# Kernel optimization log

Hardware: AMD Instinct MI355X
Metric: run time of the kernel (lower is better)

The kernel has to match this reference:

```python
import jax, jax.numpy as jnp
import numpy as np

N, E = 50000, 800000
IN_C, HID, OUT_C = 128, 128, 64
EPS = 1e-5


def layer_norm(x, gamma, beta):
    mu = jnp.mean(x, axis=-1, keepdims=True)
    var = jnp.mean(jnp.square(x - mu), axis=-1, keepdims=True)
    return (x - mu) * jax.lax.rsqrt(var + EPS) * gamma + beta


def sage_conv(h, src, dst, W_l, b_l, W_r):
    # PyG SAGEConv (aggr='mean'): out = lin_l(mean_{j in N(i)} h_j) + lin_r(h_i)
    msg = h[src]                                                   # [E, HID] gather
    s = jax.ops.segment_sum(msg, dst, num_segments=N)              # [N, HID]
    cnt = jax.ops.segment_sum(jnp.ones((src.shape[0], 1), h.dtype), dst, num_segments=N)
    mean = s / jnp.maximum(cnt, 1.0)
    return mean @ W_l + b_l + h @ W_r


def setup_inputs() -> dict:
    key = jax.random.key(0)
    ks = jax.random.split(key, 12)
    sd_in = 1.0 / np.sqrt(IN_C)
    sd_h = 1.0 / np.sqrt(HID)
    return {
        "x": jax.random.normal(ks[0], (N, IN_C), jnp.float32),
        "edge_index": jax.random.randint(ks[1], (2, E), 0, N, jnp.int32),
        "edge_attr": jax.random.normal(ks[2], (E, IN_C), jnp.float32),
        "W_ne": jax.random.uniform(ks[3], (IN_C, HID), jnp.float32, -sd_in, sd_in),
        "b_ne": jax.random.uniform(ks[4], (HID,), jnp.float32, -sd_in, sd_in),
        "W_l": jax.random.uniform(ks[5], (HID, HID), jnp.float32, -sd_h, sd_h),
        "b_l": jax.random.uniform(ks[6], (HID,), jnp.float32, -sd_h, sd_h),
        "W_r": jax.random.uniform(ks[7], (HID, HID), jnp.float32, -sd_h, sd_h),
        "gamma": jnp.ones((HID,), jnp.float32),
        "beta": jnp.zeros((HID,), jnp.float32),
        "W_lin": jax.random.uniform(ks[8], (HID, OUT_C), jnp.float32, -sd_h, sd_h),
        "b_lin": jax.random.uniform(ks[9], (OUT_C,), jnp.float32, -sd_h, sd_h),
    }


def reference(x, edge_index, edge_attr, W_ne, b_ne, W_l, b_l, W_r, gamma, beta, W_lin, b_lin):
    src, dst = edge_index[0], edge_index[1]
    # node encoder
    h = x @ W_ne + b_ne
    # pre-conv with layers[0].conv
    h = sage_conv(h, src, dst, W_l, b_l, W_r)
    # layers[0] is unfixed: LN -> ReLU -> dropout(eval=id) -> conv -> residual
    r = layer_norm(h, gamma, beta)
    r = jax.nn.relu(r)
    h = sage_conv(r, src, dst, W_l, b_l, W_r) + h
    # layers[1:] are fixed -> identity
    # final norm/act/dropout(eval=id)/lin (reuses layers[0].norm/act)
    o = jax.nn.relu(layer_norm(h, gamma, beta))
    return o @ W_lin + b_lin
```

## Files before the change

### kernel.cpp

```cpp
#include <hip/hip_runtime.h>

typedef __attribute__((ext_vector_type(8))) short bf16x8;
typedef __attribute__((ext_vector_type(4))) float f32x4;

constexpr float LN_EPS = 1e-5f;

__device__ inline ushort f2bf(float f) {
  uint u = __float_as_uint(f);
  u += 0x7FFF + ((u >> 16) & 1);
  return (ushort)(u >> 16);
}
__device__ inline float bflo(uint u) { return __uint_as_float(u << 16); }
__device__ inline float bfhi(uint u) { return __uint_as_float(u & 0xFFFF0000u); }
__device__ inline uint pk2(float lo, float hi) { return (uint)f2bf(lo) | ((uint)f2bf(hi) << 16); }

struct Params {
  const float* x; const int* ei;
  const float *W_ne, *b_ne, *W_l, *b_l, *W_r, *gamma, *beta, *W_lin, *b_lin;
  float* out;
  ushort *Qbf, *H1, *Dbf, *xbf, *WAt, *WBt, *Wlt, *Wrt, *Wlint;
  signed char* Aq;
  float* Ascale;
  float *bA, *bB;
  int *cnt, *incl, *rowptr, *cursor, *bsums, *srclist;
  int N, E, nbS, nbT, nbE;
};


__global__ __launch_bounds__(256) void k_m1(Params p) {
  __shared__ float srow[128];
  const int tid = threadIdx.x, bid = blockIdx.x;
  if (bid < p.nbE) {
    int e = bid * 256 + tid;
    if (e < p.E) atomicAdd(&p.cnt[p.ei[p.E + e]], 1);
  } else if (bid < p.nbE + 129) {
    int blk = bid - p.nbE;
    const float* src = (blk < 128) ? (p.W_ne + blk * 128) : p.b_ne;
    if (tid < 128) srow[tid] = src[tid];
    __syncthreads();
    int col = tid & 127;
    const float* Wx = (tid < 128) ? p.W_l : p.W_r;
    float acc = 0.f;
#pragma unroll 8
    for (int k = 0; k < 128; ++k) acc = fmaf(srow[k], Wx[k * 128 + col], acc);
    if (blk < 128) {
      ushort* dst = (tid < 128) ? p.WAt : p.WBt;
      dst[col * 128 + blk] = f2bf(acc);
    } else {
      float* dst = (tid < 128) ? p.bA : p.bB;
      dst[col] = acc;
    }
  } else {
    const int nx16 = p.N * 16;
    const int total = nx16 + 16384 + 16384 + 8192;
    const int i0 = (bid - (p.nbE + 129)) * 256 + tid;
    const int st = (gridDim.x - (p.nbE + 129)) * 256;
    const float4* xin = (const float4*)p.x;
    uint4* xo = (uint4*)p.xbf;
    for (int idx = i0; idx < total; idx += st) {
      if (idx < nx16) {
        float4 a = xin[2 * (size_t)idx], b = xin[2 * (size_t)idx + 1];
        uint4 v;
        v.x = pk2(a.x, a.y); v.y = pk2(a.z, a.w);
        v.z = pk2(b.x, b.y); v.w = pk2(b.z, b.w);
        xo[idx] = v;
        continue;
      }
      int t = idx - nx16;
      if (t < 16384) { p.Wlt[(t & 127) * 128 + (t >> 7)] = f2bf(p.W_l[t]); continue; }
      t -= 16384;
      if (t < 16384) { p.Wrt[(t & 127) * 128 + (t >> 7)] = f2bf(p.W_r[t]); continue; }
      t -= 16384;
      p.Wlint[(t & 63) * 128 + (t >> 6)] = f2bf(p.W_lin[t]);
    }
  }
}


template <int NCOL, int OMODE>
__device__ __forceinline__ void gemm_tile(const ushort* __restrict__ X, const ushort* __restrict__ Wt,
                                          const float* __restrict__ bias, void* __restrict__ Yv,
                                          float* __restrict__ Yscale, int M, int tile, char* ldsraw) {
  constexpr int NF = NCOL / 32;
  const int tid = threadIdx.x;
  const int wave = tid >> 6, lane = tid & 63;
  const int rbase = (wave >> 1) * 64;
  const int cbase = (wave & 1) * (NCOL / 2);
  const int lrow = lane & 15;
  const int lkb = (lane >> 4) * 8;
  const int row0 = tile * 128;

  size_t rIdx[4];
#pragma unroll
  for (int mf = 0; mf < 4; ++mf) {
    int r = row0 + rbase + mf * 16 + lrow;
    rIdx[mf] = (size_t)((r < M) ? r : (M - 1));
  }

  f32x4 acc[4][NF];
#pragma unroll
  for (int mf = 0; mf < 4; ++mf)
#pragma unroll
    for (int nf = 0; nf < NF; ++nf) acc[mf][nf] = (f32x4){0.f, 0.f, 0.f, 0.f};

#pragma unroll
  for (int ks = 0; ks < 4; ++ks) {
    bf16x8 a[4], b[NF];
#pragma unroll
    for (int mf = 0; mf < 4; ++mf)
      a[mf] = *(const bf16x8*)(X + rIdx[mf] * 128 + ks * 32 + lkb);
#pragma unroll
    for (int nf = 0; nf < NF; ++nf)
      b[nf] = *(const bf16x8*)(Wt + (size_t)(cbase + nf * 16 + lrow) * 128 + ks * 32 + lkb);
#pragma unroll
    for (int mf = 0; mf < 4; ++mf)
#pragma unroll
      for (int nf = 0; nf < NF; ++nf)
        acc[mf][nf] = __builtin_amdgcn_mfma_f32_16x16x32_bf16(a[mf], b[nf], acc[mf][nf], 0, 0, 0);
  }

  if (bias) {
#pragma unroll
    for (int nf = 0; nf < NF; ++nf) {
      float bv = bias[cbase + nf * 16 + lrow];
#pragma unroll
      for (int mf = 0; mf < 4; ++mf)
#pragma unroll
        for (int r = 0; r < 4; ++r) acc[mf][nf][r] += bv;
    }
  }

  if constexpr (OMODE == 2) {
    float (*rmaxh)[2] = (float(*)[2])ldsraw;
    signed char (*qt)[128] = (signed char(*)[128])(ldsraw + 1024);
#pragma unroll
    for (int mf = 0; mf < 4; ++mf)
#pragma unroll
      for (int r = 0; r < 4; ++r) {
        float m = 0.f;
#pragma unroll
        for (int nf = 0; nf < NF; ++nf) m = fmaxf(m, fabsf(acc[mf][nf][r]));
#pragma unroll
        for (int off = 1; off < 16; off <<= 1) m = fmaxf(m, __shfl_xor(m, off, 64));
        int lr = rbase + mf * 16 + (lane >> 4) * 4 + r;
        if (lrow == 0) rmaxh[lr][wave & 1] = m;
      }
    __syncthreads();
#pragma unroll
    for (int mf = 0; mf < 4; ++mf)
#pragma unroll
      for (int r = 0; r < 4; ++r) {
        int lr = rbase + mf * 16 + (lane >> 4) * 4 + r;
        float mx = fmaxf(rmaxh[lr][0], rmaxh[lr][1]);
        float inv = (mx > 0.f) ? 127.f / mx : 0.f;
#pragma unroll
        for (int nf = 0; nf < NF; ++nf)
          qt[lr][cbase + nf * 16 + lrow] = (signed char)__float2int_rn(acc[mf][nf][r] * inv);
      }
    __syncthreads();
    signed char* Yq = (signed char*)Yv;
    for (int idx = tid; idx < 1024; idx += 256) {
      int lr = idx >> 3, co = (idx & 7) * 16;
      int grow = row0 + lr;
      if (grow < M) *(uint4*)(Yq + (size_t)grow * 128 + co) = *(const uint4*)&qt[lr][co];
    }
    if (tid < 128) {
      int grow = row0 + tid;
      if (grow < M) Yscale[grow] = fmaxf(rmaxh[tid][0], rmaxh[tid][1]) * (1.f / 127.f);
    }
    return;
  }

#pragma unroll
  for (int nf = 0; nf < NF; ++nf) {
    int col = cbase + nf * 16 + lrow;
#pragma unroll
    for (int mf = 0; mf < 4; ++mf) {
      int growb = row0 + rbase + mf * 16 + (lane >> 4) * 4;
#pragma unroll
      for (int r = 0; r < 4; ++r) {
        int grow = growb + r;
        if (grow < M) {
          float val = acc[mf][nf][r];
          if constexpr (OMODE == 1)
            ((ushort*)Yv)[(size_t)grow * NCOL + col] = f2bf(val);
          else
            ((float*)Yv)[(size_t)grow * NCOL + col] = val;
        }
      }
    }
  }
}


__global__ __launch_bounds__(256) void k_m2(Params p) {
  __shared__ __align__(16) char qlds[1024 + 16384];
  const int bid = blockIdx.x, tid = threadIdx.x;
  if (bid < p.nbS) {
    int* sh = (int*)qlds;
    int i = bid * 256 + tid;
    int v = (i < p.N) ? p.cnt[i] : 0;
    sh[tid] = v;
    __syncthreads();
    for (int off = 1; off < 256; off <<= 1) {
      int t = (tid >= off) ? sh[tid - off] : 0;
      __syncthreads();
      sh[tid] += t;
      __syncthreads();
    }
    if (i < p.N) p.incl[i] = sh[tid];
    if (tid == 255) p.bsums[bid] = sh[255];
    return;
  }
  int job = bid - p.nbS;
  if (job < p.nbT) gemm_tile<128, 2>(p.xbf, p.WAt, p.bA, p.Aq, p.Ascale, p.N, job, qlds);
  else gemm_tile<128, 1>(p.xbf, p.WBt, p.bB, p.Qbf, nullptr, p.N, job - p.nbT, qlds);
}


__global__ __launch_bounds__(256) void k_m3(Params p) {
  __shared__ int ss[256];
  const int bid = blockIdx.x, tid = threadIdx.x;
  int v = (tid < bid) ? p.bsums[tid] : 0;
  ss[tid] = v;
  __syncthreads();
  for (int off = 128; off > 0; off >>= 1) {
    if (tid < off) ss[tid] += ss[tid + off];
    __syncthreads();
  }
  int prefix = ss[0];
  int i = bid * 256 + tid;
  if (i < p.N) {
    int inc = p.incl[i] + prefix;
    p.rowptr[i + 1] = inc;
    p.cursor[i] = inc - p.cnt[i];
  }
  if (i == 0) p.rowptr[0] = 0;
}

__global__ __launch_bounds__(256) void k_fill(Params p) {
  int e = blockIdx.x * 256 + threadIdx.x;
  if (e >= p.E) return;
  int s = p.ei[e], d = p.ei[p.E + e];
  int pos = atomicAdd(&p.cursor[d], 1);
  p.srclist[pos] = s;
}

__global__ __launch_bounds__(256) void k_gemm2(Params p) {
  __shared__ __align__(16) char qlds[1024 + 16384];
  int job = blockIdx.y * p.nbT + blockIdx.x;
  if (job < p.nbT) gemm_tile<128, 2>(p.Dbf, p.Wlt, nullptr, p.Aq, p.Ascale, p.N, job, qlds);
  else gemm_tile<128, 1>(p.Dbf, p.Wrt, nullptr, p.Qbf, nullptr, p.N, job - p.nbT, qlds);
}

__global__ __launch_bounds__(256) void k_gout(Params p) {
  gemm_tile<64, 0>(p.Dbf, p.Wlint, p.b_lin, p.out, nullptr, p.N, blockIdx.x, nullptr);
}


__device__ __forceinline__ void acc8q(uint2 u, float sc, float* a) {
  a[0] = fmaf((float)(int)(signed char)(u.x & 0xFF), sc, a[0]);
  a[1] = fmaf((float)(int)(signed char)((u.x >> 8) & 0xFF), sc, a[1]);
  a[2] = fmaf((float)(int)(signed char)((u.x >> 16) & 0xFF), sc, a[2]);
  a[3] = fmaf((float)(int)(signed char)(u.x >> 24), sc, a[3]);
  a[4] = fmaf((float)(int)(signed char)(u.y & 0xFF), sc, a[4]);
  a[5] = fmaf((float)(int)(signed char)((u.y >> 8) & 0xFF), sc, a[5]);
  a[6] = fmaf((float)(int)(signed char)((u.y >> 16) & 0xFF), sc, a[6]);
  a[7] = fmaf((float)(int)(signed char)(u.y >> 24), sc, a[7]);
}

__device__ __forceinline__ void gather_mean(const signed char* __restrict__ Pq, const float* __restrict__ Psc,
                                            const int* __restrict__ rowptr, const int* __restrict__ srclist,
                                            int w, int lane, float* a) {
  int fl = lane & 15, g4 = lane >> 4;
  int beg = rowptr[w], end = rowptr[w + 1];
  for (int base = beg; base < end; base += 64) {
    int m = end - base;
    if (m > 64) m = 64;
    int sidx = (lane < m) ? srclist[base + lane] : 0;
    for (int i = 0; i < m; i += 16) {
      int j0 = i + g4, j1 = j0 + 4, j2 = j0 + 8, j3 = j0 + 12;
      int s0 = __shfl(sidx, j0 & 63, 64);
      int s1 = __shfl(sidx, j1 & 63, 64);
      int s2 = __shfl(sidx, j2 & 63, 64);
      int s3 = __shfl(sidx, j3 & 63, 64);
      float c0 = Psc[s0], c1 = Psc[s1], c2 = Psc[s2], c3 = Psc[s3];
      uint2 u0 = *(const uint2*)(Pq + (size_t)s0 * 128 + fl * 8);
      uint2 u1 = *(const uint2*)(Pq + (size_t)s1 * 128 + fl * 8);
      uint2 u2 = *(const uint2*)(Pq + (size_t)s2 * 128 + fl * 8);
      uint2 u3 = *(const uint2*)(Pq + (size_t)s3 * 128 + fl * 8);
      if (j0 < m) acc8q(u0, c0, a);
      if (j1 < m) acc8q(u1, c1, a);
      if (j2 < m) acc8q(u2, c2, a);
      if (j3 < m) acc8q(u3, c3, a);
    }
  }
#pragma unroll
  for (int k = 0; k < 8; ++k) {
    a[k] += __shfl_xor(a[k], 16, 64);
    a[k] += __shfl_xor(a[k], 32, 64);
  }
  float inv = 1.f / fmaxf((float)(end - beg), 1.f);
#pragma unroll
  for (int k = 0; k < 8; ++k) a[k] *= inv;
}

__device__ __forceinline__ void ln_relu8(const float* h, const float* __restrict__ gamma,
                                         const float* __restrict__ beta, int fl, float* o) {
  float sum = 0.f;
#pragma unroll
  for (int k = 0; k < 8; ++k) sum += h[k];
#pragma unroll
  for (int off = 1; off < 16; off <<= 1) sum += __shfl_xor(sum, off, 64);
  float mu = sum * (1.f / 128.f);
  float s2 = 0.f;
#pragma unroll
  for (int k = 0; k < 8; ++k) { float d = h[k] - mu; s2 += d * d; }
#pragma unroll
  for (int off = 1; off < 16; off <<= 1) s2 += __shfl_xor(s2, off, 64);
  float scale = rsqrtf(s2 * (1.f / 128.f) + LN_EPS);
  float4 g0 = *(const float4*)(gamma + fl * 8);
  float4 g1 = *(const float4*)(gamma + fl * 8 + 4);
  float4 b0 = *(const float4*)(beta + fl * 8);
  float4 b1 = *(const float4*)(beta + fl * 8 + 4);
  float gg[8] = {g0.x, g0.y, g0.z, g0.w, g1.x, g1.y, g1.z, g1.w};
  float bb[8] = {b0.x, b0.y, b0.z, b0.w, b1.x, b1.y, b1.z, b1.w};
#pragma unroll
  for (int k = 0; k < 8; ++k) o[k] = fmaxf((h[k] - mu) * scale * gg[k] + bb[k], 0.f);
}

__device__ __forceinline__ uint4 pack8(const float* v) {
  uint4 u;
  u.x = pk2(v[0], v[1]); u.y = pk2(v[2], v[3]);
  u.z = pk2(v[4], v[5]); u.w = pk2(v[6], v[7]);
  return u;
}

__global__ __launch_bounds__(256) void k_agg1(Params p) {
  int w = (blockIdx.x * 256 + threadIdx.x) >> 6;
  int lane = threadIdx.x & 63;
  if (w >= p.N) return;
  int fl = lane & 15;
  float a[8] = {0.f, 0.f, 0.f, 0.f, 0.f, 0.f, 0.f, 0.f};
  gather_mean(p.Aq, p.Ascale, p.rowptr, p.srclist, w, lane, a);
  uint4 qv = ((const uint4*)p.Qbf)[(size_t)w * 16 + fl];
  float4 bl0 = *(const float4*)(p.b_l + fl * 8);
  float4 bl1 = *(const float4*)(p.b_l + fl * 8 + 4);
  float q[8] = {bflo(qv.x), bfhi(qv.x), bflo(qv.y), bfhi(qv.y), bflo(qv.z), bfhi(qv.z), bflo(qv.w), bfhi(qv.w)};
  float bl[8] = {bl0.x, bl0.y, bl0.z, bl0.w, bl1.x, bl1.y, bl1.z, bl1.w};
  float h[8];
#pragma unroll
  for (int k = 0; k < 8; ++k) h[k] = a[k] + q[k] + bl[k];
  float r[8];
  ln_relu8(h, p.gamma, p.beta, fl, r);
  if (lane < 16) {
    ((uint4*)p.H1)[(size_t)w * 16 + fl] = pack8(h);
    ((uint4*)p.Dbf)[(size_t)w * 16 + fl] = pack8(r);
  }
}

__global__ __launch_bounds__(256) void k_agg2(Params p) {
  int w = (blockIdx.x * 256 + threadIdx.x) >> 6;
  int lane = threadIdx.x & 63;
  if (w >= p.N) return;
  int fl = lane & 15;
  float a[8] = {0.f, 0.f, 0.f, 0.f, 0.f, 0.f, 0.f, 0.f};
  gather_mean(p.Aq, p.Ascale, p.rowptr, p.srclist, w, lane, a);
  uint4 vv = ((const uint4*)p.Qbf)[(size_t)w * 16 + fl];
  uint4 hv = ((const uint4*)p.H1)[(size_t)w * 16 + fl];
  float4 bl0 = *(const float4*)(p.b_l + fl * 8);
  float4 bl1 = *(const float4*)(p.b_l + fl * 8 + 4);
  float vf[8] = {bflo(vv.x), bfhi(vv.x), bflo(vv.y), bfhi(vv.y), bflo(vv.z), bfhi(vv.z), bflo(vv.w), bfhi(vv.w)};
  float hf[8] = {bflo(hv.x), bfhi(hv.x), bflo(hv.y), bfhi(hv.y), bflo(hv.z), bfhi(hv.z), bflo(hv.w), bfhi(hv.w)};
  float bl[8] = {bl0.x, bl0.y, bl0.z, bl0.w, bl1.x, bl1.y, bl1.z, bl1.w};
  float h[8];
#pragma unroll
  for (int k = 0; k < 8; ++k) h[k] = a[k] + vf[k] + bl[k] + hf[k];
  float o[8];
  ln_relu8(h, p.gamma, p.beta, fl, o);
  if (lane < 16) ((uint4*)p.Dbf)[(size_t)w * 16 + fl] = pack8(o);
}


extern "C" void kernel_launch(void* const* d_in, const int* in_sizes, int n_in,
                              void* d_out, int out_size, void* d_ws, size_t ws_size,
                              hipStream_t stream) {
  Params p;
  p.x = (const float*)d_in[0];
  p.ei = (const int*)d_in[1];
  p.W_ne = (const float*)d_in[3];
  p.b_ne = (const float*)d_in[4];
  p.W_l = (const float*)d_in[5];
  p.b_l = (const float*)d_in[6];
  p.W_r = (const float*)d_in[7];
  p.gamma = (const float*)d_in[8];
  p.beta = (const float*)d_in[9];
  p.W_lin = (const float*)d_in[10];
  p.b_lin = (const float*)d_in[11];
  p.out = (float*)d_out;

  p.N = in_sizes[0] / 128;
  p.E = in_sizes[1] / 2;
  p.nbS = (p.N + 255) / 256;
  p.nbT = (p.N + 127) / 128;
  p.nbE = (p.E + 255) / 256;

  char* w = (char*)d_ws;
  const size_t S2 = (size_t)p.N * 128 * sizeof(ushort);
  p.Qbf = (ushort*)w;    w += S2;
  p.H1 = (ushort*)w;     w += S2;
  p.Dbf = (ushort*)w;    w += S2;
  p.xbf = (ushort*)w;    w += S2;
  p.Aq = (signed char*)w;  w += (size_t)p.N * 128;
  p.Ascale = (float*)w;  w += (size_t)p.N * sizeof(float);
  p.WAt = (ushort*)w;    w += 128 * 128 * sizeof(ushort);
  p.WBt = (ushort*)w;    w += 128 * 128 * sizeof(ushort);
  p.Wlt = (ushort*)w;    w += 128 * 128 * sizeof(ushort);
  p.Wrt = (ushort*)w;    w += 128 * 128 * sizeof(ushort);
  p.Wlint = (ushort*)w;  w += 64 * 128 * sizeof(ushort);
  p.bA = (float*)w;      w += 128 * sizeof(float);
  p.bB = (float*)w;      w += 128 * sizeof(float);
  p.cnt = (int*)w;       w += (size_t)p.N * sizeof(int);
  p.incl = (int*)w;      w += (size_t)p.N * sizeof(int);
  p.rowptr = (int*)w;    w += ((size_t)p.N + 4) * sizeof(int);
  p.cursor = (int*)w;    w += (size_t)p.N * sizeof(int);
  p.bsums = (int*)w;     w += 1024 * sizeof(int);
  p.srclist = (int*)w;

  const int nbW = ((p.N * 64) + 255) / 256;

  hipMemsetAsync(p.cnt, 0, (size_t)p.N * sizeof(int), stream);
  k_m1<<<p.nbE + 129 + 1024, 256, 0, stream>>>(p);
  k_m2<<<p.nbS + 2 * p.nbT, 256, 0, stream>>>(p);
  k_m3<<<p.nbS, 256, 0, stream>>>(p);
  k_fill<<<p.nbE, 256, 0, stream>>>(p);
  k_agg1<<<nbW, 256, 0, stream>>>(p);
  k_gemm2<<<dim3(p.nbT, 2), 256, 0, stream>>>(p);
  k_agg2<<<nbW, 256, 0, stream>>>(p);
  k_gout<<<p.nbT, 256, 0, stream>>>(p);
}
```

Measured before the change: 219.1 us.

## Fuse output linear layer into second aggregation kernel

Removes the separate output GEMM kernel and computes the final 128->64 projection inside k_agg2, using the per-row LN/ReLU result staged in LDS and fp32 weights read from global memory. This avoids writing and re-reading the normalized activations and one kernel launch, and drops the bf16 W_lin transpose. The trade is scalar FMA work per row instead of matrix-core GEMM, and it also switches the output to fp32 weights.

```diff
diff --git a/kernel.cpp b/kernel.cpp
--- a/kernel.cpp
+++ b/kernel.cpp
@@ -18,7 +18,7 @@
   const float* x; const int* ei;
   const float *W_ne, *b_ne, *W_l, *b_l, *W_r, *gamma, *beta, *W_lin, *b_lin;
   float* out;
-  ushort *Qbf, *H1, *Dbf, *xbf, *WAt, *WBt, *Wlt, *Wrt, *Wlint;
+  ushort *Qbf, *H1, *Dbf, *xbf, *WAt, *WBt, *Wlt, *Wrt;
   signed char* Aq;
   float* Ascale;
   float *bA, *bB;
@@ -52,7 +52,7 @@
     }
   } else {
     const int nx16 = p.N * 16;
-    const int total = nx16 + 16384 + 16384 + 8192;
+    const int total = nx16 + 16384 + 16384;
     const int i0 = (bid - (p.nbE + 129)) * 256 + tid;
     const int st = (gridDim.x - (p.nbE + 129)) * 256;
     const float4* xin = (const float4*)p.x;
@@ -69,9 +69,7 @@
       int t = idx - nx16;
       if (t < 16384) { p.Wlt[(t & 127) * 128 + (t >> 7)] = f2bf(p.W_l[t]); continue; }
       t -= 16384;
-      if (t < 16384) { p.Wrt[(t & 127) * 128 + (t >> 7)] = f2bf(p.W_r[t]); continue; }
-      t -= 16384;
-      p.Wlint[(t & 63) * 128 + (t >> 6)] = f2bf(p.W_lin[t]);
+      p.Wrt[(t & 127) * 128 + (t >> 7)] = f2bf(p.W_r[t]);
     }
   }
 }
@@ -180,13 +178,7 @@
 #pragma unroll
       for (int r = 0; r < 4; ++r) {
         int grow = growb + r;
-        if (grow < M) {
-          float val = acc[mf][nf][r];
-          if constexpr (OMODE == 1)
-            ((ushort*)Yv)[(size_t)grow * NCOL + col] = f2bf(val);
-          else
-            ((float*)Yv)[(size_t)grow * NCOL + col] = val;
-        }
+        if (grow < M) ((ushort*)Yv)[(size_t)grow * NCOL + col] = f2bf(acc[mf][nf][r]);
       }
     }
   }
@@ -251,10 +243,6 @@
   int job = blockIdx.y * p.nbT + blockIdx.x;
   if (job < p.nbT) gemm_tile<128, 2>(p.Dbf, p.Wlt, nullptr, p.Aq, p.Ascale, p.N, job, qlds);
   else gemm_tile<128, 1>(p.Dbf, p.Wrt, nullptr, p.Qbf, nullptr, p.N, job - p.nbT, qlds);
-}
-
-__global__ __launch_bounds__(256) void k_gout(Params p) {
-  gemm_tile<64, 0>(p.Dbf, p.Wlint, p.b_lin, p.out, nullptr, p.N, blockIdx.x, nullptr);
 }
 
 
@@ -360,8 +348,10 @@
 }
 
 __global__ __launch_bounds__(256) void k_agg2(Params p) {
+  __shared__ float olds[4][128];
   int w = (blockIdx.x * 256 + threadIdx.x) >> 6;
   int lane = threadIdx.x & 63;
+  int wv = (threadIdx.x >> 6) & 3;
   if (w >= p.N) return;
   int fl = lane & 15;
   float a[8] = {0.f, 0.f, 0.f, 0.f, 0.f, 0.f, 0.f, 0.f};
@@ -378,7 +368,20 @@
   for (int k = 0; k < 8; ++k) h[k] = a[k] + vf[k] + bl[k] + hf[k];
   float o[8];
   ln_relu8(h, p.gamma, p.beta, fl, o);
-  if (lane < 16) ((uint4*)p.Dbf)[(size_t)w * 16 + fl] = pack8(o);
+  if (lane < 16) {
+#pragma unroll
+    for (int k = 0; k < 8; ++k) olds[wv][fl * 8 + k] = o[k];
+  }
+  const float* Wl = p.W_lin + lane;
+  float a0 = 0.f, a1 = 0.f, a2 = 0.f, a3 = 0.f;
+#pragma unroll 8
+  for (int k = 0; k < 128; k += 4) {
+    a0 = fmaf(olds[wv][k], Wl[(size_t)k * 64], a0);
+    a1 = fmaf(olds[wv][k + 1], Wl[(size_t)(k + 1) * 64], a1);
+    a2 = fmaf(olds[wv][k + 2], Wl[(size_t)(k + 2) * 64], a2);
+    a3 = fmaf(olds[wv][k + 3], Wl[(size_t)(k + 3) * 64], a3);
+  }
+  p.out[(size_t)w * 64 + lane] = p.b_lin[lane] + ((a0 + a1) + (a2 + a3));
 }
 
 
@@ -417,7 +420,6 @@
   p.WBt = (ushort*)w;    w += 128 * 128 * sizeof(ushort);
   p.Wlt = (ushort*)w;    w += 128 * 128 * sizeof(ushort);
   p.Wrt = (ushort*)w;    w += 128 * 128 * sizeof(ushort);
-  p.Wlint = (ushort*)w;  w += 64 * 128 * sizeof(ushort);
   p.bA = (float*)w;      w += 128 * sizeof(float);
   p.bB = (float*)w;      w += 128 * sizeof(float);
   p.cnt = (int*)w;       w += (size_t)p.N * sizeof(int);
@@ -437,5 +439,4 @@
   k_agg1<<<nbW, 256, 0, stream>>>(p);
   k_gemm2<<<dim3(p.nbT, 2), 256, 0, stream>>>(p);
   k_agg2<<<nbW, 256, 0, stream>>>(p);
-  k_gout<<<p.nbT, 256, 0, stream>>>(p);
-}
+}
```

Result: slower. 252.4 us (+15.2%).
